# Optimization experiments

Measured on AMD Instinct MI355X. Metric: run time of the kernel, lower is better.

## Reference

```python
import jax, jax.numpy as jnp
import numpy as np

T_ITERS = 48  # number of unrolled PDHG iterations (init kwarg T)


def _grad3(u):
    """Forward-difference gradient with circular BC.
    u: (P, 1, X, Y, T) -> (P, 3, X, Y, T).
    conv with kernel (0,-1,1) + circular pad == roll(v,-1,axis) - v."""
    v = u[:, 0]
    return jnp.stack([jnp.roll(v, -1, axis=a) - v for a in (1, 2, 3)], axis=1)


def _grad3_adj(q):
    """Adjoint (negative divergence) with circular BC.
    q: (P, 3, X, Y, T) -> (P, 1, X, Y, T)."""
    out = sum(jnp.roll(q[:, d], 1, axis=d + 1) - q[:, d] for d in range(3))
    return out[:, None]


def setup_inputs() -> dict:
    key = jax.random.key(0)
    k1, k2 = jax.random.split(key)
    x = jax.random.normal(k1, (2, 1, 160, 160, 16), dtype=jnp.float32)
    # positive per-voxel regularization map, one per gradient direction
    lambda_map = jax.random.uniform(k2, (2, 3, 160, 160, 16), dtype=jnp.float32)
    return {"x": x, "lambda_map": lambda_map}


def reference(x, lambda_map):
    # op_norm_AHA = 1, op_norm_GHG = sqrt(12) -> L = sqrt(1 + 12)
    L = jnp.sqrt(jnp.asarray(13.0, x.dtype))
    s10 = jax.nn.sigmoid(jnp.asarray(10.0, x.dtype))  # sigmoid of init value 10.0
    sigma = s10 / L
    tau = s10 / L
    theta = s10

    xnoisy = x
    p = x
    q = jnp.zeros((x.shape[0], 3) + x.shape[2:], dtype=x.dtype)
    x0 = x
    xbar = x

    def step(carry, _):
        p, q, x0, xbar = carry
        p = (p + sigma * (xbar - xnoisy)) / (1.0 + sigma)
        q = jnp.clip(q + sigma * _grad3(xbar), -lambda_map, lambda_map)
        x1 = x0 - tau * p - tau * _grad3_adj(q)
        xbar = x1 + theta * (x1 - x0)
        return (p, q, x1, xbar), None

    (p, q, x1, xbar), _ = jax.lax.scan(step, (p, q, x0, xbar), None, length=T_ITERS)
    return x1
```

## Files before the change

### kernel.cpp

```cpp
#include <hip/hip_runtime.h>
#include <math.h>

#define XDIM 160
#define YDIM 160
#define TDIM 16
#define NB 2
#define T_ITERS 48
#define TILE 10
#define R1S 16
#define R0S 18
#define TPT (XDIM / TILE)
#define NTHR 512
#define NGRP (T_ITERS / 4)
#define NLEAF 8

constexpr int VOL  = XDIM * YDIM * TDIM;
constexpr int NX   = NB * VOL;
constexpr int NBLK = NB * TPT * TPT;

typedef _Float16 hreal;
typedef _Float16 half4 __attribute__((ext_vector_type(4)));

__device__ __forceinline__ float clampl(float v, float l) {
    return fminf(fmaxf(v, -l), l);
}
__device__ __forceinline__ int wrap(int v) {
    return v < 0 ? v + XDIM : (v >= XDIM ? v - XDIM : v);
}
__device__ __forceinline__ void ld4(const float* p, float* d) {
    float4 v = *(const float4*)p;
    d[0] = v.x; d[1] = v.y; d[2] = v.z; d[3] = v.w;
}
__device__ __forceinline__ void st4(float* p, const float* s) {
    *(float4*)p = make_float4(s[0], s[1], s[2], s[3]);
}
__device__ __forceinline__ void h2f4(const hreal* p, float* d) {
    half4 v = *(const half4*)p;
    d[0] = (float)v.x; d[1] = (float)v.y; d[2] = (float)v.z; d[3] = (float)v.w;
}
__device__ __forceinline__ float qrot_up(float x) {
    return __int_as_float(__builtin_amdgcn_update_dpp(
        0, __float_as_int(x), 0x39, 0xF, 0xF, true));
}
__device__ __forceinline__ float qrot_dn(float x) {
    return __int_as_float(__builtin_amdgcn_update_dpp(
        0, __float_as_int(x), 0x93, 0xF, 0xF, true));
}

__device__ __forceinline__ void grid_barrier(unsigned* bar) {
    __threadfence();
    __syncthreads();
    if (threadIdx.x == 0) {
        unsigned s = __hip_atomic_load(bar + 129, __ATOMIC_RELAXED,
                                       __HIP_MEMORY_SCOPE_AGENT);
        const unsigned leaf = (blockIdx.x & (NLEAF - 1)) * 16;
        const unsigned per  = NBLK / NLEAF;
        bool done = false;
        if (__hip_atomic_fetch_add(bar + leaf, 1u, __ATOMIC_ACQ_REL,
                                   __HIP_MEMORY_SCOPE_AGENT) == per - 1u) {
            __hip_atomic_store(bar + leaf, 0u, __ATOMIC_RELAXED,
                               __HIP_MEMORY_SCOPE_AGENT);
            if (__hip_atomic_fetch_add(bar + 128, 1u, __ATOMIC_ACQ_REL,
                                       __HIP_MEMORY_SCOPE_AGENT) == NLEAF - 1u) {
                __hip_atomic_store(bar + 128, 0u, __ATOMIC_RELAXED,
                                   __HIP_MEMORY_SCOPE_AGENT);
                __hip_atomic_store(bar + 129, s + 1u, __ATOMIC_RELEASE,
                                   __HIP_MEMORY_SCOPE_AGENT);
                done = true;
            }
        }
        if (!done) {
            for (unsigned it = 0; it < (1u << 22); ++it) {
                if (__hip_atomic_load(bar + 129, __ATOMIC_RELAXED,
                                      __HIP_MEMORY_SCOPE_AGENT) != s) break;
                __builtin_amdgcn_s_sleep(4);
            }
        }
    }
    __syncthreads();
    __threadfence();
}

__global__ __launch_bounds__(256) void init_kernel(
    const float* __restrict__ x, const float* __restrict__ lam,
    float* __restrict__ pA, float* __restrict__ xA,
    hreal* __restrict__ xbAh, hreal* __restrict__ qAh,
    hreal* __restrict__ lamh, hreal* __restrict__ xnh,
    unsigned* __restrict__ bar)
{
    int i = blockIdx.x * blockDim.x + threadIdx.x;
    if (i < NX) {
        float v = x[i];
        pA[i] = v; xA[i] = v;
        xbAh[i] = (hreal)v;
        xnh[i]  = (hreal)v;
    }
    if (i < 3 * NX) {
        qAh[i]  = (hreal)0.f;
        lamh[i] = (hreal)lam[i];
    }
    if (bar && i < 130) bar[i] = 0u;
}

__global__ __launch_bounds__(NTHR, 4) void pd_persist(
    const hreal* __restrict__ xnh, const hreal* __restrict__ lamh,
    float* __restrict__ pA, float* __restrict__ pB,
    float* __restrict__ xA, float* __restrict__ xB,
    hreal* __restrict__ xbA, hreal* __restrict__ xbB,
    hreal* __restrict__ qA, hreal* __restrict__ qB,
    unsigned* __restrict__ bar,
    float sigma, float inv1ps, float tau, float theta)
{
    __shared__ float xbS[R0S * R0S * TDIM];
    __shared__ float q0S[(R1S + 1) * R1S * TDIM];
    __shared__ float q1S[R1S * (R1S + 1) * TDIM];

    const int tid = threadIdx.x;
    const int b   = blockIdx.x / (TPT * TPT);
    const int rem = blockIdx.x % (TPT * TPT);
    const int X0  = (rem / TPT) * TILE;
    const int Y0  = (rem % TPT) * TILE;
    const int xbase = b * VOL, qbase = b * 3 * VOL;
    const int t0 = (tid & 3) * 4;

    float p[2][4], xv[2][4], xb[2][4], q0[2][4], q1[2][4], q2[2][4];
    half4 XNr[2], L0r[2], L1r[2], L2r[2];

    #pragma unroll
    for (int m = 0; m < 2; ++m) {
        int line = 128 * m + (tid >> 2);
        int lx = line >> 4, ly = line & 15;
        int gx = wrap(X0 - 3 + lx), gy = wrap(Y0 - 3 + ly);
        int off  = xbase + (gx * YDIM + gy) * TDIM + t0;
        int qoff = qbase + (gx * YDIM + gy) * TDIM + t0;
        XNr[m] = *(const half4*)(xnh + off);
        L0r[m] = *(const half4*)(lamh + qoff);
        L1r[m] = *(const half4*)(lamh + qoff + VOL);
        L2r[m] = *(const half4*)(lamh + qoff + 2 * VOL);
    }
    half4 LRr;
    if (tid < 64) {
        int rly = tid >> 2;
        LRr = *(const half4*)(lamh + qbase +
              (wrap(X0 - 4) * YDIM + wrap(Y0 - 3 + rly)) * TDIM + t0);
    } else if (tid < 128) {
        int rlx = (tid - 64) >> 2;
        LRr = *(const half4*)(lamh + qbase + VOL +
              (wrap(X0 - 3 + rlx) * YDIM + wrap(Y0 - 4)) * TDIM + t0);
    }

    #pragma unroll 1
    for (int g = 0; g < NGRP; ++g) {
        const bool e = (g & 1) == 0;
        const bool first = (g == 0);
        const float* __restrict__ pIn  = e ? pA : pB;
        float* __restrict__ pOut       = e ? pB : pA;
        const float* __restrict__ xIn  = e ? xA : xB;
        float* __restrict__ xOut       = e ? xB : xA;
        const hreal* __restrict__ xbIn = e ? xbA : xbB;
        hreal* __restrict__ xbOut      = e ? xbB : xbA;
        const hreal* __restrict__ qIn  = e ? qA : qB;
        hreal* __restrict__ qOut       = e ? qB : qA;

        for (int s = tid; s < R0S * R0S * 4; s += NTHR) {
            int sq = s & 3, ln = s >> 2;
            int rx = ln / R0S, ry = ln % R0S;
            if (!first && rx >= 4 && rx < 14 && ry >= 4 && ry < 14) continue;
            int gx = wrap(X0 - 4 + rx), gy = wrap(Y0 - 4 + ry);
            float v[4];
            h2f4(xbIn + xbase + (gx * YDIM + gy) * TDIM + sq * 4, v);
            st4(xbS + ln * TDIM + sq * 4, v);
        }
        for (int s = tid; s < 17 * 16 * 4; s += NTHR) {
            int sq = s & 3, ln = s >> 2;
            int sx = ln / 16, sy = ln % 16;
            if (!first && sx >= 3 && sx < 14 && sy >= 3 && sy < 13) continue;
            int gx = wrap(X0 - 4 + sx), gy = wrap(Y0 - 3 + sy);
            float v[4];
            h2f4(qIn + qbase + (gx * YDIM + gy) * TDIM + sq * 4, v);
            st4(q0S + ln * TDIM + sq * 4, v);
        }
        for (int s = tid; s < 16 * 17 * 4; s += NTHR) {
            int sq = s & 3, ln = s >> 2;
            int sx = ln / 17, sy = ln % 17;
            if (!first && sx >= 3 && sx < 13 && sy >= 3 && sy < 14) continue;
            int gx = wrap(X0 - 3 + sx), gy = wrap(Y0 - 4 + sy);
            float v[4];
            h2f4(qIn + qbase + VOL + (gx * YDIM + gy) * TDIM + sq * 4, v);
            st4(q1S + ln * TDIM + sq * 4, v);
        }

        #pragma unroll
        for (int m = 0; m < 2; ++m) {
            int line = 128 * m + (tid >> 2);
            int lx = line >> 4, ly = line & 15;
            bool c = lx >= 3 && lx < 13 && ly >= 3 && ly < 13;
            if (first || !c) {
                int gx = wrap(X0 - 3 + lx), gy = wrap(Y0 - 3 + ly);
                int off  = xbase + (gx * YDIM + gy) * TDIM + t0;
                int qoff = qbase + (gx * YDIM + gy) * TDIM + t0;
                ld4(pIn + off, p[m]);
                ld4(xIn + off, xv[m]);
                h2f4(qIn + qoff + 2 * VOL, q2[m]);
            }
        }
        __syncthreads();
        #pragma unroll
        for (int m = 0; m < 2; ++m) {
            int line = 128 * m + (tid >> 2);
            int lx = line >> 4, ly = line & 15;
            bool c = lx >= 3 && lx < 13 && ly >= 3 && ly < 13;
            if (first || !c)
                ld4(xbS + ((lx + 1) * R0S + (ly + 1)) * TDIM + t0, xb[m]);
        }

        #pragma unroll
        for (int k = 1; k <= 4; ++k) {
            const int lo = k - 1, hi = 17 - k;

            if (k == 1) {
                if (tid < 64) {
                    int rly = tid >> 2;
                    float qr[4], xbc[4], xpx[4];
                    ld4(q0S + (0 * R1S + rly) * TDIM + t0, qr);
                    ld4(xbS + (0 * R0S + (rly + 1)) * TDIM + t0, xbc);
                    ld4(xbS + (1 * R0S + (rly + 1)) * TDIM + t0, xpx);
                    #pragma unroll
                    for (int j = 0; j < 4; ++j)
                        qr[j] = clampl(qr[j] + sigma * (xpx[j] - xbc[j]), (float)LRr[j]);
                    st4(q0S + (0 * R1S + rly) * TDIM + t0, qr);
                } else if (tid < 128) {
                    int rlx = (tid - 64) >> 2;
                    float qr[4], xbc[4], xpy[4];
                    ld4(q1S + (rlx * 17 + 0) * TDIM + t0, qr);
                    ld4(xbS + ((rlx + 1) * R0S + 0) * TDIM + t0, xbc);
                    ld4(xbS + ((rlx + 1) * R0S + 1) * TDIM + t0, xpy);
                    #pragma unroll
                    for (int j = 0; j < 4; ++j)
                        qr[j] = clampl(qr[j] + sigma * (xpy[j] - xbc[j]), (float)LRr[j]);
                    st4(q1S + (rlx * 17 + 0) * TDIM + t0, qr);
                }
            }

            #pragma unroll
            for (int m = 0; m < 2; ++m) {
                int line = 128 * m + (tid >> 2);
                int lx = line >> 4, ly = line & 15;
                bool inX = (lx >= lo && lx < hi), inY = (ly >= lo && ly < hi);
                bool aq0 = inY && (lx >= lo - 1) && (lx < hi);
                bool aq1 = inX && (ly >= lo - 1) && (ly < hi);
                bool ax  = inX && inY;

                if (k == 1) {
                    bool c = lx >= 3 && lx < 13 && ly >= 3 && ly < 13;
                    if (first || !c) {
                        ld4(q0S + ((lx + 1) * R1S + ly) * TDIM + t0, q0[m]);
                        ld4(q1S + (lx * 17 + (ly + 1)) * TDIM + t0, q1[m]);
                    }
                }
                if (aq0) {
                    float xpx[4];
                    ld4(xbS + ((lx + 2) * R0S + (ly + 1)) * TDIM + t0, xpx);
                    #pragma unroll
                    for (int j = 0; j < 4; ++j)
                        q0[m][j] = clampl(q0[m][j] + sigma * (xpx[j] - xb[m][j]),
                                          (float)L0r[m][j]);
                    st4(q0S + ((lx + 1) * R1S + ly) * TDIM + t0, q0[m]);
                }
                if (aq1) {
                    float xpy[4];
                    ld4(xbS + ((lx + 1) * R0S + (ly + 2)) * TDIM + t0, xpy);
                    #pragma unroll
                    for (int j = 0; j < 4; ++j)
                        q1[m][j] = clampl(q1[m][j] + sigma * (xpy[j] - xb[m][j]),
                                          (float)L1r[m][j]);
                    st4(q1S + (lx * 17 + (ly + 1)) * TDIM + t0, q1[m]);
                }
                if (ax) {
                    float xb_tp = qrot_up(xb[m][0]);
                    #pragma unroll
                    for (int j = 0; j < 4; ++j) {
                        float gt = ((j < 3) ? xb[m][j + 1] : xb_tp) - xb[m][j];
                        q2[m][j] = clampl(q2[m][j] + sigma * gt, (float)L2r[m][j]);
                        p[m][j]  = (p[m][j] + sigma * (xb[m][j] - (float)XNr[m][j]))
                                   * inv1ps;
                    }
                }
            }
            __syncthreads();

            #pragma unroll
            for (int m = 0; m < 2; ++m) {
                int line = 128 * m + (tid >> 2);
                int lx = line >> 4, ly = line & 15;
                bool ax = (lx >= lo && lx < hi && ly >= lo && ly < hi);
                if (ax) {
                    float q0b[4], q1b[4];
                    ld4(q0S + (lx * R1S + ly) * TDIM + t0, q0b);
                    ld4(q1S + (lx * 17 + ly) * TDIM + t0, q1b);
                    float q2tm = qrot_dn(q2[m][3]);
                    #pragma unroll
                    for (int j = 0; j < 4; ++j) {
                        float q2p = (j == 0) ? q2tm : q2[m][j - 1];
                        float div = (q0b[j] - q0[m][j]) + (q1b[j] - q1[m][j])
                                  + (q2p - q2[m][j]);
                        float xnew = xv[m][j] - tau * (p[m][j] + div);
                        xb[m][j] = xnew + theta * (xnew - xv[m][j]);
                        xv[m][j] = xnew;
                    }
                    st4(xbS + ((lx + 1) * R0S + (ly + 1)) * TDIM + t0, xb[m]);
                }
            }
            if (k < 4) __syncthreads();
        }

        #pragma unroll
        for (int m = 0; m < 2; ++m) {
            int line = 128 * m + (tid >> 2);
            int lx = line >> 4, ly = line & 15;
            if (lx >= 3 && lx < 13 && ly >= 3 && ly < 13) {
                int gx = X0 + lx - 3, gy = Y0 + ly - 3;
                int off  = xbase + (gx * YDIM + gy) * TDIM + t0;
                int qoff = qbase + (gx * YDIM + gy) * TDIM + t0;
                st4(pOut + off, p[m]);
                st4(xOut + off, xv[m]);
                half4 h;
                h.x = (hreal)xb[m][0]; h.y = (hreal)xb[m][1];
                h.z = (hreal)xb[m][2]; h.w = (hreal)xb[m][3];
                *(half4*)(xbOut + off) = h;
                h.x = (hreal)q0[m][0]; h.y = (hreal)q0[m][1];
                h.z = (hreal)q0[m][2]; h.w = (hreal)q0[m][3];
                *(half4*)(qOut + qoff) = h;
                h.x = (hreal)q1[m][0]; h.y = (hreal)q1[m][1];
                h.z = (hreal)q1[m][2]; h.w = (hreal)q1[m][3];
                *(half4*)(qOut + qoff + VOL) = h;
                h.x = (hreal)q2[m][0]; h.y = (hreal)q2[m][1];
                h.z = (hreal)q2[m][2]; h.w = (hreal)q2[m][3];
                *(half4*)(qOut + qoff + 2 * VOL) = h;
            }
        }

        if (g + 1 < NGRP) grid_barrier(bar);
    }
}

__global__ __launch_bounds__(NTHR, 4) void pd_step4(
    const hreal* __restrict__ xnh, const hreal* __restrict__ lamh,
    const float* __restrict__ pIn, float* __restrict__ pOut,
    const float* __restrict__ xIn, float* __restrict__ xOut,
    const hreal* __restrict__ xbIn, hreal* __restrict__ xbOut,
    const hreal* __restrict__ qIn, hreal* __restrict__ qOut,
    float sigma, float inv1ps, float tau, float theta)
{
    __shared__ float xbS[R0S * R0S * TDIM];
    __shared__ float q0S[(R1S + 1) * R1S * TDIM];
    __shared__ float q1S[R1S * (R1S + 1) * TDIM];

    const int tid = threadIdx.x;
    const int b   = blockIdx.x / (TPT * TPT);
    const int rem = blockIdx.x % (TPT * TPT);
    const int X0  = (rem / TPT) * TILE;
    const int Y0  = (rem % TPT) * TILE;
    const int xbase = b * VOL, qbase = b * 3 * VOL;

    const int qd = tid & 3, t0 = qd * 4;
    const int lane  = tid & 63;
    const int upSrc = (lane & 60) | ((lane + 1) & 3);
    const int dnSrc = (lane & 60) | ((lane + 3) & 3);

    for (int s = tid; s < R0S * R0S * 4; s += NTHR) {
        int sq = s & 3, ln = s >> 2;
        int rx = ln / R0S, ry = ln % R0S;
        int gx = wrap(X0 - 4 + rx), gy = wrap(Y0 - 4 + ry);
        float v[4];
        h2f4(xbIn + xbase + (gx * YDIM + gy) * TDIM + sq * 4, v);
        st4(xbS + ln * TDIM + sq * 4, v);
    }
    for (int s = tid; s < 17 * 16 * 4; s += NTHR) {
        int sq = s & 3, ln = s >> 2;
        int sx = ln / 16, sy = ln % 16;
        int gx = wrap(X0 - 4 + sx), gy = wrap(Y0 - 3 + sy);
        float v[4];
        h2f4(qIn + qbase + (gx * YDIM + gy) * TDIM + sq * 4, v);
        st4(q0S + ln * TDIM + sq * 4, v);
    }
    for (int s = tid; s < 16 * 17 * 4; s += NTHR) {
        int sq = s & 3, ln = s >> 2;
        int sx = ln / 17, sy = ln % 17;
        int gx = wrap(X0 - 3 + sx), gy = wrap(Y0 - 4 + sy);
        float v[4];
        h2f4(qIn + qbase + VOL + (gx * YDIM + gy) * TDIM + sq * 4, v);
        st4(q1S + ln * TDIM + sq * 4, v);
    }

    float p[2][4], xv[2][4], xb[2][4], q0[2][4], q1[2][4], q2[2][4];
    half4 XNr[2], L0r[2], L1r[2], L2r[2];
    #pragma unroll
    for (int m = 0; m < 2; ++m) {
        int line = 128 * m + (tid >> 2);
        int lx = line >> 4, ly = line & 15;
        int gx = wrap(X0 - 3 + lx), gy = wrap(Y0 - 3 + ly);
        int off  = xbase + (gx * YDIM + gy) * TDIM + t0;
        int qoff = qbase + (gx * YDIM + gy) * TDIM + t0;
        ld4(pIn + off, p[m]);
        ld4(xIn + off, xv[m]);
        h2f4(qIn + qoff + 2 * VOL, q2[m]);
        XNr[m] = *(const half4*)(xnh + off);
        L0r[m] = *(const half4*)(lamh + qoff);
        L1r[m] = *(const half4*)(lamh + qoff + VOL);
        L2r[m] = *(const half4*)(lamh + qoff + 2 * VOL);
    }

    half4 LRr;
    if (tid < 64) {
        int rly = tid >> 2;
        LRr = *(const half4*)(lamh + qbase +
              (wrap(X0 - 4) * YDIM + wrap(Y0 - 3 + rly)) * TDIM + t0);
    } else if (tid < 128) {
        int rlx = (tid - 64) >> 2;
        LRr = *(const half4*)(lamh + qbase + VOL +
              (wrap(X0 - 3 + rlx) * YDIM + wrap(Y0 - 4)) * TDIM + t0);
    }

    __syncthreads();

    #pragma unroll
    for (int m = 0; m < 2; ++m) {
        int line = 128 * m + (tid >> 2);
        int lx = line >> 4, ly = line & 15;
        ld4(xbS + ((lx + 1) * R0S + (ly + 1)) * TDIM + t0, xb[m]);
    }

    #pragma unroll
    for (int k = 1; k <= 4; ++k) {
        const int lo = k - 1, hi = 17 - k;

        if (k == 1) {
            if (tid < 64) {
                int rly = tid >> 2;
                float qr[4], xbc[4], xpx[4];
                ld4(q0S + (0 * R1S + rly) * TDIM + t0, qr);
                ld4(xbS + (0 * R0S + (rly + 1)) * TDIM + t0, xbc);
                ld4(xbS + (1 * R0S + (rly + 1)) * TDIM + t0, xpx);
                #pragma unroll
                for (int j = 0; j < 4; ++j)
                    qr[j] = clampl(qr[j] + sigma * (xpx[j] - xbc[j]), (float)LRr[j]);
                st4(q0S + (0 * R1S + rly) * TDIM + t0, qr);
            } else if (tid < 128) {
                int rlx = (tid - 64) >> 2;
                float qr[4], xbc[4], xpy[4];
                ld4(q1S + (rlx * 17 + 0) * TDIM + t0, qr);
                ld4(xbS + ((rlx + 1) * R0S + 0) * TDIM + t0, xbc);
                ld4(xbS + ((rlx + 1) * R0S + 1) * TDIM + t0, xpy);
                #pragma unroll
                for (int j = 0; j < 4; ++j)
                    qr[j] = clampl(qr[j] + sigma * (xpy[j] - xbc[j]), (float)LRr[j]);
                st4(q1S + (rlx * 17 + 0) * TDIM + t0, qr);
            }
        }

        #pragma unroll
        for (int m = 0; m < 2; ++m) {
            int line = 128 * m + (tid >> 2);
            int lx = line >> 4, ly = line & 15;
            bool inX = (lx >= lo && lx < hi), inY = (ly >= lo && ly < hi);
            bool aq0 = inY && (lx >= lo - 1) && (lx < hi);
            bool aq1 = inX && (ly >= lo - 1) && (ly < hi);
            bool ax  = inX && inY;

            if (k == 1) {
                ld4(q0S + ((lx + 1) * R1S + ly) * TDIM + t0, q0[m]);
                ld4(q1S + (lx * 17 + (ly + 1)) * TDIM + t0, q1[m]);
            }
            if (aq0) {
                float xpx[4];
                ld4(xbS + ((lx + 2) * R0S + (ly + 1)) * TDIM + t0, xpx);
                #pragma unroll
                for (int j = 0; j < 4; ++j)
                    q0[m][j] = clampl(q0[m][j] + sigma * (xpx[j] - xb[m][j]),
                                      (float)L0r[m][j]);
                st4(q0S + ((lx + 1) * R1S + ly) * TDIM + t0, q0[m]);
            }
            if (aq1) {
                float xpy[4];
                ld4(xbS + ((lx + 1) * R0S + (ly + 2)) * TDIM + t0, xpy);
                #pragma unroll
                for (int j = 0; j < 4; ++j)
                    q1[m][j] = clampl(q1[m][j] + sigma * (xpy[j] - xb[m][j]),
                                      (float)L1r[m][j]);
                st4(q1S + (lx * 17 + (ly + 1)) * TDIM + t0, q1[m]);
            }
            if (ax) {
                float xb_tp = __shfl(xb[m][0], upSrc, 64);
                #pragma unroll
                for (int j = 0; j < 4; ++j) {
                    float gt = ((j < 3) ? xb[m][j + 1] : xb_tp) - xb[m][j];
                    q2[m][j] = clampl(q2[m][j] + sigma * gt, (float)L2r[m][j]);
                    p[m][j]  = (p[m][j] + sigma * (xb[m][j] - (float)XNr[m][j]))
                               * inv1ps;
                }
            }
        }
        __syncthreads();

        #pragma unroll
        for (int m = 0; m < 2; ++m) {
            int line = 128 * m + (tid >> 2);
            int lx = line >> 4, ly = line & 15;
            bool ax = (lx >= lo && lx < hi && ly >= lo && ly < hi);
            if (ax) {
                float q0b[4], q1b[4];
                ld4(q0S + (lx * R1S + ly) * TDIM + t0, q0b);
                ld4(q1S + (lx * 17 + ly) * TDIM + t0, q1b);
                float q2tm = __shfl(q2[m][3], dnSrc, 64);
                #pragma unroll
                for (int j = 0; j < 4; ++j) {
                    float q2p = (j == 0) ? q2tm : q2[m][j - 1];
                    float div = (q0b[j] - q0[m][j]) + (q1b[j] - q1[m][j])
                              + (q2p - q2[m][j]);
                    float xnew = xv[m][j] - tau * (p[m][j] + div);
                    xb[m][j] = xnew + theta * (xnew - xv[m][j]);
                    xv[m][j] = xnew;
                }
                if (k < 4)
                    st4(xbS + ((lx + 1) * R0S + (ly + 1)) * TDIM + t0, xb[m]);
            }
        }
        if (k < 4) __syncthreads();
    }

    #pragma unroll
    for (int m = 0; m < 2; ++m) {
        int line = 128 * m + (tid >> 2);
        int lx = line >> 4, ly = line & 15;
        if (lx >= 3 && lx < 13 && ly >= 3 && ly < 13) {
            int gx = X0 + lx - 3, gy = Y0 + ly - 3;
            int off  = xbase + (gx * YDIM + gy) * TDIM + t0;
            int qoff = qbase + (gx * YDIM + gy) * TDIM + t0;
            st4(pOut + off, p[m]);
            st4(xOut + off, xv[m]);
            half4 h;
            h.x = (hreal)xb[m][0]; h.y = (hreal)xb[m][1];
            h.z = (hreal)xb[m][2]; h.w = (hreal)xb[m][3];
            *(half4*)(xbOut + off) = h;
            h.x = (hreal)q0[m][0]; h.y = (hreal)q0[m][1];
            h.z = (hreal)q0[m][2]; h.w = (hreal)q0[m][3];
            *(half4*)(qOut + qoff) = h;
            h.x = (hreal)q1[m][0]; h.y = (hreal)q1[m][1];
            h.z = (hreal)q1[m][2]; h.w = (hreal)q1[m][3];
            *(half4*)(qOut + qoff + VOL) = h;
            h.x = (hreal)q2[m][0]; h.y = (hreal)q2[m][1];
            h.z = (hreal)q2[m][2]; h.w = (hreal)q2[m][3];
            *(half4*)(qOut + qoff + 2 * VOL) = h;
        }
    }
}

extern "C" void kernel_launch(void* const* d_in, const int* in_sizes, int n_in,
                              void* d_out, int out_size, void* d_ws, size_t ws_size,
                              hipStream_t stream) {
    const float* x   = (const float*)d_in[0];
    const float* lam = (const float*)d_in[1];
    float* out = (float*)d_out;
    float* ws  = (float*)d_ws;

    float* pA  = ws;
    float* pB  = ws + (size_t)NX;
    float* xBb = ws + (size_t)2 * NX;
    float* xAb = out;
    hreal* hb  = (hreal*)(ws + (size_t)3 * NX);
    hreal* xbAh = hb;
    hreal* xbBh = hb + (size_t)NX;
    hreal* qAh  = hb + (size_t)2 * NX;
    hreal* qBh  = hb + (size_t)5 * NX;
    hreal* lamh = hb + (size_t)8 * NX;
    hreal* xnh  = hb + (size_t)11 * NX;
    unsigned* bar = (unsigned*)(ws + (size_t)9 * NX);

    const size_t ws_need = (size_t)9 * NX * sizeof(float) + 130 * sizeof(unsigned);

    const double s10 = 1.0 / (1.0 + exp(-10.0));
    const double L   = sqrt(13.0);
    float sigma  = (float)(s10 / L);
    float tau    = sigma;
    float theta  = (float)s10;
    float inv1ps = (float)(1.0 / (1.0 + s10 / L));

    static int persist_ok = -1;
    if (persist_ok < 0) {
        int nb = 0;
        hipError_t oe = hipOccupancyMaxActiveBlocksPerMultiprocessor(
            &nb, pd_persist, NTHR, 0);
        persist_ok = (oe == hipSuccess && nb >= 2) ? 1 : 0;
        (void)hipGetLastError();
    }
    const bool use_persist = persist_ok == 1 && ws_size >= ws_need;

    init_kernel<<<(3 * NX + 255) / 256, 256, 0, stream>>>(
        x, lam, pA, xAb, xbAh, qAh, lamh, xnh, use_persist ? bar : nullptr);

    if (use_persist) {
        pd_persist<<<NBLK, NTHR, 0, stream>>>(
            xnh, lamh, pA, pB, xAb, xBb, xbAh, xbBh, qAh, qBh, bar,
            sigma, inv1ps, tau, theta);
    } else {
        for (int j = 0; j < NGRP; ++j) {
            const bool e = (j & 1) == 0;
            pd_step4<<<NBLK, NTHR, 0, stream>>>(
                xnh, lamh,
                e ? pA : pB,   e ? pB : pA,
                e ? xAb : xBb, e ? xBb : xAb,
                e ? xbAh : xbBh, e ? xbBh : xbAh,
                e ? qAh : qBh,  e ? qBh : qAh,
                sigma, inv1ps, tau, theta);
        }
    }
}
```

Before: 254.5 us.

## Replace grid barrier with neighbor flag sync and skip unneeded interior stores

Removes the tree-based global grid barrier from the persistent kernel. Each block now publishes a per-block progress flag and waits only on its 8 neighboring tiles before loading halos for the next group of iterations. Interior outputs that neighbors never read (p/x centre, and the inner xbar/q core) are no longer written back, and the final group stores only x. This cuts global synchronization latency and store traffic. In exchange, correctness now depends on the halo-region reasoning and on the acquire/release ordering between neighboring blocks.

```diff
diff --git a/kernel.cpp b/kernel.cpp
--- a/kernel.cpp
+++ b/kernel.cpp
@@ -12,7 +12,7 @@
 #define TPT (XDIM / TILE)
 #define NTHR 512
 #define NGRP (T_ITERS / 4)
-#define NLEAF 8
+#define FLAG_STRIDE 16
 
 constexpr int VOL  = XDIM * YDIM * TDIM;
 constexpr int NX   = NB * VOL;
@@ -27,6 +27,9 @@
 __device__ __forceinline__ int wrap(int v) {
     return v < 0 ? v + XDIM : (v >= XDIM ? v - XDIM : v);
 }
+__device__ __forceinline__ int wrapT(int v) {
+    return v < 0 ? v + TPT : (v >= TPT ? v - TPT : v);
+}
 __device__ __forceinline__ void ld4(const float* p, float* d) {
     float4 v = *(const float4*)p;
     d[0] = v.x; d[1] = v.y; d[2] = v.z; d[3] = v.w;
@@ -45,40 +48,6 @@
 __device__ __forceinline__ float qrot_dn(float x) {
     return __int_as_float(__builtin_amdgcn_update_dpp(
         0, __float_as_int(x), 0x93, 0xF, 0xF, true));
-}
-
-__device__ __forceinline__ void grid_barrier(unsigned* bar) {
-    __threadfence();
-    __syncthreads();
-    if (threadIdx.x == 0) {
-        unsigned s = __hip_atomic_load(bar + 129, __ATOMIC_RELAXED,
-                                       __HIP_MEMORY_SCOPE_AGENT);
-        const unsigned leaf = (blockIdx.x & (NLEAF - 1)) * 16;
-        const unsigned per  = NBLK / NLEAF;
-        bool done = false;
-        if (__hip_atomic_fetch_add(bar + leaf, 1u, __ATOMIC_ACQ_REL,
-                                   __HIP_MEMORY_SCOPE_AGENT) == per - 1u) {
-            __hip_atomic_store(bar + leaf, 0u, __ATOMIC_RELAXED,
-                               __HIP_MEMORY_SCOPE_AGENT);
-            if (__hip_atomic_fetch_add(bar + 128, 1u, __ATOMIC_ACQ_REL,
-                                       __HIP_MEMORY_SCOPE_AGENT) == NLEAF - 1u) {
-                __hip_atomic_store(bar + 128, 0u, __ATOMIC_RELAXED,
-                                   __HIP_MEMORY_SCOPE_AGENT);
-                __hip_atomic_store(bar + 129, s + 1u, __ATOMIC_RELEASE,
-                                   __HIP_MEMORY_SCOPE_AGENT);
-                done = true;
-            }
-        }
-        if (!done) {
-            for (unsigned it = 0; it < (1u << 22); ++it) {
-                if (__hip_atomic_load(bar + 129, __ATOMIC_RELAXED,
-                                      __HIP_MEMORY_SCOPE_AGENT) != s) break;
-                __builtin_amdgcn_s_sleep(4);
-            }
-        }
-    }
-    __syncthreads();
-    __threadfence();
 }
 
 __global__ __launch_bounds__(256) void init_kernel(
@@ -86,7 +55,7 @@
     float* __restrict__ pA, float* __restrict__ xA,
     hreal* __restrict__ xbAh, hreal* __restrict__ qAh,
     hreal* __restrict__ lamh, hreal* __restrict__ xnh,
-    unsigned* __restrict__ bar)
+    unsigned* __restrict__ flags)
 {
     int i = blockIdx.x * blockDim.x + threadIdx.x;
     if (i < NX) {
@@ -99,7 +68,7 @@
         qAh[i]  = (hreal)0.f;
         lamh[i] = (hreal)lam[i];
     }
-    if (bar && i < 130) bar[i] = 0u;
+    if (flags && i < NBLK * FLAG_STRIDE) flags[i] = 0u;
 }
 
 __global__ __launch_bounds__(NTHR, 4) void pd_persist(
@@ -108,7 +77,7 @@
     float* __restrict__ xA, float* __restrict__ xB,
     hreal* __restrict__ xbA, hreal* __restrict__ xbB,
     hreal* __restrict__ qA, hreal* __restrict__ qB,
-    unsigned* __restrict__ bar,
+    unsigned* __restrict__ flags,
     float sigma, float inv1ps, float tau, float theta)
 {
     __shared__ float xbS[R0S * R0S * TDIM];
@@ -116,12 +85,23 @@
     __shared__ float q1S[R1S * (R1S + 1) * TDIM];
 
     const int tid = threadIdx.x;
-    const int b   = blockIdx.x / (TPT * TPT);
-    const int rem = blockIdx.x % (TPT * TPT);
-    const int X0  = (rem / TPT) * TILE;
-    const int Y0  = (rem % TPT) * TILE;
+    const int bid = blockIdx.x;
+    const int b   = bid / (TPT * TPT);
+    const int rem = bid % (TPT * TPT);
+    const int tx  = rem / TPT, ty = rem % TPT;
+    const int X0  = tx * TILE;
+    const int Y0  = ty * TILE;
     const int xbase = b * VOL, qbase = b * 3 * VOL;
     const int t0 = (tid & 3) * 4;
+
+    const unsigned* nbFlag = nullptr;
+    if (tid < 8) {
+        const int dxs[8] = {-1,-1,-1, 0, 0, 1, 1, 1};
+        const int dys[8] = {-1, 0, 1,-1, 1,-1, 0, 1};
+        int nx = wrapT(tx + dxs[tid]);
+        int ny = wrapT(ty + dys[tid]);
+        nbFlag = flags + (b * TPT * TPT + nx * TPT + ny) * FLAG_STRIDE;
+    }
 
     float p[2][4], xv[2][4], xb[2][4], q0[2][4], q1[2][4], q2[2][4];
     half4 XNr[2], L0r[2], L1r[2], L2r[2];
@@ -153,6 +133,7 @@
     for (int g = 0; g < NGRP; ++g) {
         const bool e = (g & 1) == 0;
         const bool first = (g == 0);
+        const bool fin   = (g == NGRP - 1);
         const float* __restrict__ pIn  = e ? pA : pB;
         float* __restrict__ pOut       = e ? pB : pA;
         const float* __restrict__ xIn  = e ? xA : xB;
@@ -161,6 +142,20 @@
         hreal* __restrict__ xbOut      = e ? xbB : xbA;
         const hreal* __restrict__ qIn  = e ? qA : qB;
         hreal* __restrict__ qOut       = e ? qB : qA;
+
+        if (!first) {
+            if (tid < 8) {
+                const unsigned tgt = (unsigned)g;
+                for (unsigned it = 0; it < (1u << 22); ++it) {
+                    if (__hip_atomic_load(nbFlag, __ATOMIC_ACQUIRE,
+                                          __HIP_MEMORY_SCOPE_AGENT) >= tgt)
+                        break;
+                    __builtin_amdgcn_s_sleep(1);
+                }
+            }
+            __syncthreads();
+            __threadfence();
+        }
 
         for (int s = tid; s < R0S * R0S * 4; s += NTHR) {
             int sq = s & 3, ln = s >> 2;
@@ -319,28 +314,45 @@
             int line = 128 * m + (tid >> 2);
             int lx = line >> 4, ly = line & 15;
             if (lx >= 3 && lx < 13 && ly >= 3 && ly < 13) {
-                int gx = X0 + lx - 3, gy = Y0 + ly - 3;
+                int ox = lx - 3, oy = ly - 3;
+                int gx = X0 + ox, gy = Y0 + oy;
                 int off  = xbase + (gx * YDIM + gy) * TDIM + t0;
                 int qoff = qbase + (gx * YDIM + gy) * TDIM + t0;
-                st4(pOut + off, p[m]);
-                st4(xOut + off, xv[m]);
-                half4 h;
-                h.x = (hreal)xb[m][0]; h.y = (hreal)xb[m][1];
-                h.z = (hreal)xb[m][2]; h.w = (hreal)xb[m][3];
-                *(half4*)(xbOut + off) = h;
-                h.x = (hreal)q0[m][0]; h.y = (hreal)q0[m][1];
-                h.z = (hreal)q0[m][2]; h.w = (hreal)q0[m][3];
-                *(half4*)(qOut + qoff) = h;
-                h.x = (hreal)q1[m][0]; h.y = (hreal)q1[m][1];
-                h.z = (hreal)q1[m][2]; h.w = (hreal)q1[m][3];
-                *(half4*)(qOut + qoff + VOL) = h;
-                h.x = (hreal)q2[m][0]; h.y = (hreal)q2[m][1];
-                h.z = (hreal)q2[m][2]; h.w = (hreal)q2[m][3];
-                *(half4*)(qOut + qoff + 2 * VOL) = h;
-            }
-        }
-
-        if (g + 1 < NGRP) grid_barrier(bar);
+                if (fin) {
+                    st4(xOut + off, xv[m]);
+                } else {
+                    bool px_skip = (ox >= 3 && ox < 7 && oy >= 3 && oy < 7);
+                    bool q_skip  = (ox >= 4 && ox < 6 && oy >= 4 && oy < 6);
+                    if (!px_skip) {
+                        st4(pOut + off, p[m]);
+                        st4(xOut + off, xv[m]);
+                    }
+                    if (!q_skip) {
+                        half4 h;
+                        h.x = (hreal)xb[m][0]; h.y = (hreal)xb[m][1];
+                        h.z = (hreal)xb[m][2]; h.w = (hreal)xb[m][3];
+                        *(half4*)(xbOut + off) = h;
+                        h.x = (hreal)q0[m][0]; h.y = (hreal)q0[m][1];
+                        h.z = (hreal)q0[m][2]; h.w = (hreal)q0[m][3];
+                        *(half4*)(qOut + qoff) = h;
+                        h.x = (hreal)q1[m][0]; h.y = (hreal)q1[m][1];
+                        h.z = (hreal)q1[m][2]; h.w = (hreal)q1[m][3];
+                        *(half4*)(qOut + qoff + VOL) = h;
+                        h.x = (hreal)q2[m][0]; h.y = (hreal)q2[m][1];
+                        h.z = (hreal)q2[m][2]; h.w = (hreal)q2[m][3];
+                        *(half4*)(qOut + qoff + 2 * VOL) = h;
+                    }
+                }
+            }
+        }
+
+        if (!fin) {
+            __threadfence();
+            __syncthreads();
+            if (tid == 0)
+                __hip_atomic_store(flags + bid * FLAG_STRIDE, (unsigned)(g + 1),
+                                   __ATOMIC_RELEASE, __HIP_MEMORY_SCOPE_AGENT);
+        }
     }
 }
 
@@ -575,9 +587,10 @@
     hreal* qBh  = hb + (size_t)5 * NX;
     hreal* lamh = hb + (size_t)8 * NX;
     hreal* xnh  = hb + (size_t)11 * NX;
-    unsigned* bar = (unsigned*)(ws + (size_t)9 * NX);
-
-    const size_t ws_need = (size_t)9 * NX * sizeof(float) + 130 * sizeof(unsigned);
+    unsigned* flags = (unsigned*)(ws + (size_t)9 * NX);
+
+    const size_t ws_need = (size_t)9 * NX * sizeof(float)
+                         + (size_t)NBLK * FLAG_STRIDE * sizeof(unsigned);
 
     const double s10 = 1.0 / (1.0 + exp(-10.0));
     const double L   = sqrt(13.0);
@@ -597,11 +610,11 @@
     const bool use_persist = persist_ok == 1 && ws_size >= ws_need;
 
     init_kernel<<<(3 * NX + 255) / 256, 256, 0, stream>>>(
-        x, lam, pA, xAb, xbAh, qAh, lamh, xnh, use_persist ? bar : nullptr);
+        x, lam, pA, xAb, xbAh, qAh, lamh, xnh, use_persist ? flags : nullptr);
 
     if (use_persist) {
         pd_persist<<<NBLK, NTHR, 0, stream>>>(
-            xnh, lamh, pA, pB, xAb, xBb, xbAh, xbBh, qAh, qBh, bar,
+            xnh, lamh, pA, pB, xAb, xBb, xbAh, xbBh, qAh, qBh, flags,
             sigma, inv1ps, tau, theta);
     } else {
         for (int j = 0; j < NGRP; ++j) {
```

Result: no change. 252.4 us (-0.9%).
